# Kernel tuning notes

Hardware: AMD Instinct MI355X
Metric: run time of the kernel (lower is better)

Reference implementation:

```python
import jax, jax.numpy as jnp
import numpy as np

N_QUBITS = 10
DEPTH = 6
NUM_CLASSES = 16
BATCH = 65536

# PennyLane default.qubit convention: wire 0 is the most significant bit of the
# computational-basis index. State kept as (B, 2**n) complex64.

def _rot(state, w, n, c, s, is_ry):
    """Apply RX (is_ry=False) or RY (is_ry=True) with cos/sin of half-angle c,s
    (broadcastable to (B,1,1)) on wire w of an n-qubit batched state."""
    B = state.shape[0]
    st = state.reshape(B, 1 << w, 2, 1 << (n - 1 - w))
    a0, a1 = st[:, :, 0, :], st[:, :, 1, :]
    if is_ry:
        n0 = c * a0 - s * a1
        n1 = s * a0 + c * a1
    else:  # RX: [[c, -i s], [-i s, c]]
        n0 = c * a0 - 1j * s * a1
        n1 = -1j * s * a0 + c * a1
    return jnp.stack([n0, n1], axis=2).reshape(B, -1)


def _cz(state, w, n):
    """CZ on wires (w, w+1): negate amplitudes where both bits are 1."""
    B = state.shape[0]
    st = state.reshape(B, 1 << w, 2, 2, 1 << (n - 2 - w))
    st = st.at[:, :, 1, 1, :].multiply(-1.0)
    return st.reshape(B, -1)


def _expval_z(probs, w, n):
    B = probs.shape[0]
    p = probs.reshape(B, 1 << w, 2, 1 << (n - 1 - w))
    return (p[:, :, 0, :] - p[:, :, 1, :]).sum(axis=(1, 2))


def setup_inputs() -> dict:
    key = jax.random.key(0)
    k1, k2, k3, k4 = jax.random.split(key, 4)
    x = jax.random.normal(k1, (BATCH, N_QUBITS), dtype=jnp.float32)
    params = jax.random.normal(k2, (DEPTH, N_QUBITS), dtype=jnp.float32)
    bound = 1.0 / np.sqrt(N_QUBITS)
    w_cls = jax.random.uniform(k3, (NUM_CLASSES, N_QUBITS), minval=-bound, maxval=bound, dtype=jnp.float32)
    b_cls = jax.random.uniform(k4, (NUM_CLASSES,), minval=-bound, maxval=bound, dtype=jnp.float32)
    return {"x": x, "params": params, "w_cls": w_cls, "b_cls": b_cls}


def reference(x, params, w_cls, b_cls):
    B, n = x.shape[0], N_QUBITS
    state = jnp.zeros((B, 1 << n), dtype=jnp.complex64).at[:, 0].set(1.0)
    # Data encoding: RX(x[:, q]) on wire q (per-sample angles).
    for q in range(n):
        half = x[:, q] * 0.5
        c = jnp.cos(half)[:, None, None]
        s = jnp.sin(half)[:, None, None]
        state = _rot(state, q, n, c, s, is_ry=False)
    # Variational ansatz: per layer, RY(params[d, q]) then CZ ladder.
    for d in range(DEPTH):
        for q in range(n):
            half = params[d, q] * 0.5
            state = _rot(state, q, n, jnp.cos(half), jnp.sin(half), is_ry=True)
        for q in range(n - 1):
            state = _cz(state, q, n)
    probs = state.real ** 2 + state.imag ** 2  # (B, 2**n)
    exp = jnp.stack([_expval_z(probs, q, n) for q in range(n)], axis=1)  # (B, n)
    return exp @ w_cls.T + b_cls
```

## Files before the change

kernel.cpp:

```cpp
#include <hip/hip_runtime.h>
#include <math.h>


typedef unsigned int u32;
typedef _Float16 h2 __attribute__((ext_vector_type(2)));

constexpr int NQ = 10;
constexpr int NCLS = 16;
constexpr u32 SGN  = 0x80000000u;
constexpr u32 SGN2 = 0x80008000u;

__device__ __forceinline__ float i2f(int i) { return __builtin_bit_cast(float, i); }
__device__ __forceinline__ int   f2i(float f) { return __builtin_bit_cast(int, f); }
__device__ __forceinline__ u32   f2u(float f) { return __builtin_bit_cast(u32, f); }
__device__ __forceinline__ float u2f(u32 u)   { return __builtin_bit_cast(float, u); }
__device__ __forceinline__ u32   h2u(h2 v)    { return __builtin_bit_cast(u32, v); }
__device__ __forceinline__ h2    u2h(u32 u)   { return __builtin_bit_cast(h2, u); }

__device__ __forceinline__ h2 fma2(h2 a, h2 b, h2 c) {
    return __builtin_elementwise_fma(a, b, c);
}

template<int SWZ>
__device__ __forceinline__ h2 swzh(h2 v) {
    return u2h((u32)__builtin_amdgcn_ds_swizzle(__builtin_bit_cast(int, v), SWZ));
}
template<int SWZ>
__device__ __forceinline__ float swzf(float v) {
    return i2f(__builtin_amdgcn_ds_swizzle(f2i(v), SWZ));
}

constexpr int SW1 = 0x041F;
constexpr int SW2 = 0x081F;
constexpr int SW4 = 0x101F;
constexpr int SW8 = 0x201F;
#define GBC(q) (0x10 | ((q) << 5))

template<int SWZ>
__device__ __forceinline__ void cross_ry(h2 (&st)[64], h2 ts) {
#pragma unroll
    for (int r = 0; r < 64; ++r) st[r] = fma2(ts, swzh<SWZ>(st[r]), st[r]);
}

template<int B, int NB>
__device__ __forceinline__ void local_ry(h2 (&st)[64], h2 t) {
#pragma unroll
    for (int r0 = 0; r0 < 64; ++r0) {
        if ((r0 & (1 << B)) == 0) {
            const int r1 = r0 | (1 << B);
            const h2 a0 = st[r0], a1 = st[r1];
            if ((__builtin_popcount(r0 & NB) & 1) == 0) {
                st[r0] = fma2(t, -a1, a0);
                st[r1] = fma2(t,  a0, a1);
            } else {
                st[r0] = fma2(t,  a1, a0);
                st[r1] = fma2(t, -a0, a1);
            }
        }
    }
}

struct Sgn { u32 n0, m0, n1, m1, n2, m2, n3, m3, g4; };

template<bool MOD, bool GS>
__device__ __forceinline__ void ry_layer(h2 (&st)[64], const u32* __restrict__ tw,
                                         int base, int gi, const Sgn& sg) {
    { const h2 ts = u2h(tw[base + 0] ^ (MOD ? sg.m0 : sg.n0)); cross_ry<SW8>(st, ts); }
    { const h2 ts = u2h(tw[base + 1] ^ (MOD ? sg.m1 : sg.n1)); cross_ry<SW4>(st, ts); }
    { const h2 ts = u2h(tw[base + 2] ^ (MOD ? sg.m2 : sg.n2)); cross_ry<SW2>(st, ts); }
    {
        const h2 ts = u2h(tw[base + 3] ^ (MOD ? sg.m3 : sg.n3));
        if constexpr (MOD) {
            const h2 th = u2h(h2u(ts) ^ SGN2);
#pragma unroll
            for (int r = 0; r < 32; ++r)  st[r] = fma2(ts, swzh<SW1>(st[r]), st[r]);
#pragma unroll
            for (int r = 32; r < 64; ++r) st[r] = fma2(th, swzh<SW1>(st[r]), st[r]);
        } else {
            cross_ry<SW1>(st, ts);
        }
    }
    { const h2 t = u2h(tw[base + 4] ^ (MOD ? sg.g4 : 0u));
      local_ry<5, MOD ? 0x10 : 0>(st, t); }
    local_ry<4, MOD ? 0x28 : 0>(st, u2h(tw[base + 5]));
    local_ry<3, MOD ? 0x14 : 0>(st, u2h(tw[base + 6]));
    local_ry<2, MOD ? 0x0A : 0>(st, u2h(tw[base + 7]));
    local_ry<1, MOD ? 0x05 : 0>(st, u2h(tw[base + 8]));
    local_ry<0, MOD ? 0x02 : 0>(st, u2h(tw[base + 9]));
    if constexpr (GS) {
        const h2 g = u2h(tw[gi]);
#pragma unroll
        for (int r = 0; r < 64; ++r) st[r] = g * st[r];
    }
}

__global__ void __launch_bounds__(64) qnn_prep(const float* __restrict__ params,
                                               u32* __restrict__ ws) {
    const int l = threadIdx.x;
    if (l < 60) {
        float s, c;
        __sincosf(params[l] * 0.5f, &s, &c);
        const float t = s / c;
        const h2 t2 = { (_Float16)t, (_Float16)t };
        ws[l] = h2u(t2);
    }
    if (l < 3) {
        float g = 1.f;
        for (int k = 0; k < 20; ++k) g *= __cosf(params[l * 20 + k] * 0.5f);
        const h2 g2 = { (_Float16)g, (_Float16)g };
        ws[60 + l] = h2u(g2);
    }
}

__global__ void __launch_bounds__(256) qnn_kernel(
    const float* __restrict__ x,
    const u32*   __restrict__ tw,
    const float* __restrict__ w_cls,
    const float* __restrict__ b_cls,
    float* __restrict__ out,
    int batch)
{
    const int lane = threadIdx.x & 63;
    const int wid  = threadIdx.x >> 6;
    const int wave = blockIdx.x * (blockDim.x >> 6) + wid;
    const int g    = lane & 15;
    const int b    = wave * 4 + (lane >> 4);

    float cx, sx;
    { const int q = (g < NQ) ? g : 0; __sincosf(x[b * NQ + q] * 0.5f, &sx, &cx); }

#define BCQ(Q) const float c##Q = swzf<GBC(Q)>(cx), s##Q = swzf<GBC(Q)>(sx);
    BCQ(0) BCQ(1) BCQ(2) BCQ(3) BCQ(4) BCQ(5) BCQ(6) BCQ(7) BCQ(8) BCQ(9)
#undef BCQ

    Sgn sg;
    sg.n0 = (g & 8) ? 0 : SGN2;  sg.m0 = sg.n0 ^ ((g & 4) ? SGN2 : 0);
    sg.n1 = (g & 4) ? 0 : SGN2;  sg.m1 = sg.n1 ^ ((((g >> 3) ^ (g >> 1)) & 1) ? SGN2 : 0);
    sg.n2 = (g & 2) ? 0 : SGN2;  sg.m2 = sg.n2 ^ ((((g >> 2) ^ g) & 1) ? SGN2 : 0);
    sg.n3 = (g & 1) ? 0 : SGN2;  sg.m3 = sg.n3 ^ (((g >> 1) & 1) ? SGN2 : 0);
    sg.g4 = (g & 1) ? SGN2 : 0;

    float F = ((g >> 3) & 1 ? s0 : c0) * ((g >> 2) & 1 ? s1 : c1)
            * ((g >> 1) & 1 ? s2 : c2) * ((g & 1) ? s3 : c3);
    const int lpar = __popc(g & (g >> 1) & 0x7) & 1;
    F = u2f(f2u(F) ^ (u32(lpar) << 31));
    const float s4m = (g & 1) ? -s4 : s4;
    float uu[8], vv[8];
    {
        const float a0 = F * c4, a1 = F * s4m;
        const float b0 = c5, b1 = s5;
        const float t00 = a0 * b0, t01 = a0 * b1, t10 = a1 * b0, t11 = a1 * b1;
        uu[0] = t00 * c6; uu[1] = t00 * s6; uu[2] = t01 * c6; uu[3] = t01 * s6;
        uu[4] = t10 * c6; uu[5] = t10 * s6; uu[6] = t11 * c6; uu[7] = t11 * s6;
        const float p00 = c7 * c8, p01 = c7 * s8, p10 = s7 * c8, p11 = s7 * s8;
        vv[0] = p00 * c9; vv[1] = p00 * s9; vv[2] = p01 * c9; vv[3] = p01 * s9;
        vv[4] = p10 * c9; vv[5] = p10 * s9; vv[6] = p11 * c9; vv[7] = p11 * s9;
    }
    const int kl = __popc(g) & 3;
    const float pa = (kl == 0) ? 1.f : ((kl == 2) ? -1.f : 0.f);
    const float pb = (kl == 1) ? -1.f : ((kl == 3) ? 1.f : 0.f);
    const float phx[4] = {pa, pb, -pa, -pb};
    const float phy[4] = {pb, -pa, -pb, pa};

    h2 st[64];
#pragma unroll
    for (int r = 0; r < 64; ++r) {
        const float Ar = uu[r >> 3] * vv[r & 7];
        const int j = ((__popc(r) & 3) + 2 * (__popc(r & (r >> 1) & 0x1F) & 1)) & 3;
        st[r] = __builtin_bit_cast(h2, __builtin_amdgcn_cvt_pkrtz(Ar * phx[j], Ar * phy[j]));
    }

    ry_layer<true , false>(st, tw,  0,  0, sg);
    ry_layer<false, true >(st, tw, 10, 60, sg);
    ry_layer<true , false>(st, tw, 20,  0, sg);
    ry_layer<false, true >(st, tw, 30, 61, sg);
    ry_layer<true , false>(st, tw, 40,  0, sg);
    ry_layer<false, true >(st, tw, 50, 62, sg);

    float f4 = 0.f, f5 = 0.f, f6 = 0.f, f7 = 0.f, f8 = 0.f, f9 = 0.f, pt = 0.f;
#pragma unroll
    for (int i = 0; i < 8; ++i) {
        float p[8];
#pragma unroll
        for (int j = 0; j < 8; ++j)
            p[j] = __builtin_amdgcn_fdot2(st[8*i + j], st[8*i + j], 0.f, false);
        const float a0 = p[0] + p[1], a1 = p[2] + p[3];
        const float a2 = p[4] + p[5], a3 = p[6] + p[7];
        f9 += (p[0] - p[1]) + (p[2] - p[3]) + (p[4] - p[5]) + (p[6] - p[7]);
        const float b0 = a0 + a1, b1 = a2 + a3;
        f8 += (a0 - a1) + (a2 - a3);
        const float c = b0 + b1;
        f7 += b0 - b1;
        f6 += (i & 1) ? -c : c;
        f5 += (i & 2) ? -c : c;
        f4 += (i & 4) ? -c : c;
        pt += c;
    }

    h2 p45 = __builtin_bit_cast(h2, __builtin_amdgcn_cvt_pkrtz(f4, f5));
    h2 p67 = __builtin_bit_cast(h2, __builtin_amdgcn_cvt_pkrtz(f6, f7));
    h2 p89 = __builtin_bit_cast(h2, __builtin_amdgcn_cvt_pkrtz(f8, f9));
    p45 += swzh<SW1>(p45);  p67 += swzh<SW1>(p67);  p89 += swzh<SW1>(p89);
    p45 += swzh<SW2>(p45);  p67 += swzh<SW2>(p67);  p89 += swzh<SW2>(p89);
    p45 += swzh<SW4>(p45);  p67 += swzh<SW4>(p67);  p89 += swzh<SW4>(p89);
    p45 += swzh<SW8>(p45);  p67 += swzh<SW8>(p67);  p89 += swzh<SW8>(p89);
    const float g4v = (float)p45[0], g5v = (float)p45[1];
    const float g6v = (float)p67[0], g7v = (float)p67[1];
    const float g8v = (float)p89[0], g9v = (float)p89[1];

    float v = pt;
    {
        float p;
        p = swzf<SW1>(v);  v = p + u2f(f2u(v) ^ ((g & 1) ? SGN : 0u));
        p = swzf<SW2>(v);  v = p + u2f(f2u(v) ^ ((g & 2) ? SGN : 0u));
        p = swzf<SW4>(v);  v = p + u2f(f2u(v) ^ ((g & 4) ? SGN : 0u));
        p = swzf<SW8>(v);  v = p + u2f(f2u(v) ^ ((g & 8) ? SGN : 0u));
    }
    const float e0 = swzf<GBC(8)>(v);
    const float e1 = swzf<GBC(4)>(v);
    const float e2 = swzf<GBC(2)>(v);
    const float e3 = swzf<GBC(1)>(v);

    {
        const float* wr = w_cls + g * NQ;
        float dot = e0 * wr[0];
        dot = fmaf(e1,  wr[1], dot);
        dot = fmaf(e2,  wr[2], dot);
        dot = fmaf(e3,  wr[3], dot);
        dot = fmaf(g4v, wr[4], dot);
        dot = fmaf(g5v, wr[5], dot);
        dot = fmaf(g6v, wr[6], dot);
        dot = fmaf(g7v, wr[7], dot);
        dot = fmaf(g8v, wr[8], dot);
        dot = fmaf(g9v, wr[9], dot);
        out[b * NCLS + g] = dot + b_cls[g];
    }
}

extern "C" void kernel_launch(void* const* d_in, const int* in_sizes, int n_in,
                              void* d_out, int out_size, void* d_ws, size_t ws_size,
                              hipStream_t stream) {
    const float* x      = (const float*)d_in[0];
    const float* params = (const float*)d_in[1];
    const float* w_cls  = (const float*)d_in[2];
    const float* b_cls  = (const float*)d_in[3];
    float* out = (float*)d_out;
    u32*   ws  = (u32*)d_ws;

    const int batch = in_sizes[0] / NQ;
    const int WAVES_PER_BLOCK = 4;
    const int ELEMS_PER_BLOCK = WAVES_PER_BLOCK * 4;

    hipLaunchKernelGGL(qnn_prep, dim3(1), dim3(64), 0, stream, params, ws);

    dim3 block(64 * WAVES_PER_BLOCK);
    dim3 grid(batch / ELEMS_PER_BLOCK);
    hipLaunchKernelGGL(qnn_kernel, grid, block, 0, stream,
                       x, (const u32*)ws, w_cls, b_cls, out, batch);
}
```

Before: 160.0 us.

## Fold first RY layer into product-state encoding and merge normalization scales

The first variational RY layer acts on a product state before any CZ, so it is folded analytically into each qubit's complex single-qubit amplitudes (RY·RX computed per lane from precomputed cos/sin of params). This removes one full ry_layer pass over the 64-register state. In exchange the initial state build uses complex multiplies instead of real ones. The gain normalisations of the later layers are regrouped: one fp16 scale is applied inside a layer and the rest is applied as a squared fp32 factor on the probabilities, which changes rounding and fp16 range behaviour.

```diff
diff --git a/kernel.cpp b/kernel.cpp
--- a/kernel.cpp
+++ b/kernel.cpp
@@ -35,6 +35,12 @@
 constexpr int SW4 = 0x101F;
 constexpr int SW8 = 0x201F;
 #define GBC(q) (0x10 | ((q) << 5))
+
+struct c32 { float re, im; };
+__device__ __forceinline__ c32 cmul(c32 a, c32 b) {
+    return { fmaf(a.re, b.re, -(a.im * b.im)),
+             fmaf(a.re, b.im,  a.im * b.re) };
+}
 
 template<int SWZ>
 __device__ __forceinline__ void cross_ry(h2 (&st)[64], h2 ts) {
@@ -104,11 +110,20 @@
         const h2 t2 = { (_Float16)t, (_Float16)t };
         ws[l] = h2u(t2);
     }
-    if (l < 3) {
-        float g = 1.f;
-        for (int k = 0; k < 20; ++k) g *= __cosf(params[l * 20 + k] * 0.5f);
-        const h2 g2 = { (_Float16)g, (_Float16)g };
-        ws[60 + l] = h2u(g2);
+    if (l < 10) {
+        float s, c;
+        __sincosf(params[l] * 0.5f, &s, &c);
+        ws[64 + 2*l]     = f2u(c);
+        ws[64 + 2*l + 1] = f2u(s);
+    }
+    if (l == 0) {
+        float gA = 1.f;
+        for (int k = 10; k < 30; ++k) gA *= __cosf(params[k] * 0.5f);
+        const h2 g2 = { (_Float16)gA, (_Float16)gA };
+        ws[60] = h2u(g2);
+        float gB = 1.f;
+        for (int k = 30; k < 60; ++k) gB *= __cosf(params[k] * 0.5f);
+        ws[61] = f2u(gB * gB);
     }
 }
 
@@ -126,12 +141,20 @@
     const int g    = lane & 15;
     const int b    = wave * 4 + (lane >> 4);
 
-    float cx, sx;
-    { const int q = (g < NQ) ? g : 0; __sincosf(x[b * NQ + q] * 0.5f, &sx, &cx); }
-
-#define BCQ(Q) const float c##Q = swzf<GBC(Q)>(cx), s##Q = swzf<GBC(Q)>(sx);
-    BCQ(0) BCQ(1) BCQ(2) BCQ(3) BCQ(4) BCQ(5) BCQ(6) BCQ(7) BCQ(8) BCQ(9)
-#undef BCQ
+    float Are, Aim, Bre, Bim;
+    {
+        const int q = (g < NQ) ? g : 0;
+        float cxe, sxe;
+        __sincosf(x[b * NQ + q] * 0.5f, &sxe, &cxe);
+        const float ct = u2f(tw[64 + 2*q]), st_ = u2f(tw[64 + 2*q + 1]);
+        Are = ct * cxe;  Aim = st_ * sxe;
+        Bre = st_ * cxe; Bim = -(ct * sxe);
+    }
+
+#define BCW(Q) const float Ar##Q = swzf<GBC(Q)>(Are), Ai##Q = swzf<GBC(Q)>(Aim), \
+                           Br##Q = swzf<GBC(Q)>(Bre), Bi##Q = swzf<GBC(Q)>(Bim);
+    BCW(0) BCW(1) BCW(2) BCW(3) BCW(4) BCW(5) BCW(6) BCW(7) BCW(8) BCW(9)
+#undef BCW
 
     Sgn sg;
     sg.n0 = (g & 8) ? 0 : SGN2;  sg.m0 = sg.n0 ^ ((g & 4) ? SGN2 : 0);
@@ -140,42 +163,59 @@
     sg.n3 = (g & 1) ? 0 : SGN2;  sg.m3 = sg.n3 ^ (((g >> 1) & 1) ? SGN2 : 0);
     sg.g4 = (g & 1) ? SGN2 : 0;
 
-    float F = ((g >> 3) & 1 ? s0 : c0) * ((g >> 2) & 1 ? s1 : c1)
-            * ((g >> 1) & 1 ? s2 : c2) * ((g & 1) ? s3 : c3);
-    const int lpar = __popc(g & (g >> 1) & 0x7) & 1;
-    F = u2f(f2u(F) ^ (u32(lpar) << 31));
-    const float s4m = (g & 1) ? -s4 : s4;
-    float uu[8], vv[8];
-    {
-        const float a0 = F * c4, a1 = F * s4m;
-        const float b0 = c5, b1 = s5;
-        const float t00 = a0 * b0, t01 = a0 * b1, t10 = a1 * b0, t11 = a1 * b1;
-        uu[0] = t00 * c6; uu[1] = t00 * s6; uu[2] = t01 * c6; uu[3] = t01 * s6;
-        uu[4] = t10 * c6; uu[5] = t10 * s6; uu[6] = t11 * c6; uu[7] = t11 * s6;
-        const float p00 = c7 * c8, p01 = c7 * s8, p10 = s7 * c8, p11 = s7 * s8;
-        vv[0] = p00 * c9; vv[1] = p00 * s9; vv[2] = p01 * c9; vv[3] = p01 * s9;
-        vv[4] = p10 * c9; vv[5] = p10 * s9; vv[6] = p11 * c9; vv[7] = p11 * s9;
-    }
-    const int kl = __popc(g) & 3;
-    const float pa = (kl == 0) ? 1.f : ((kl == 2) ? -1.f : 0.f);
-    const float pb = (kl == 1) ? -1.f : ((kl == 3) ? 1.f : 0.f);
-    const float phx[4] = {pa, pb, -pa, -pb};
-    const float phy[4] = {pb, -pa, -pb, pa};
+    const c32 w0 = (g & 8) ? c32{Br0, Bi0} : c32{Ar0, Ai0};
+    const c32 w1 = (g & 4) ? c32{Br1, Bi1} : c32{Ar1, Ai1};
+    const c32 w2 = (g & 2) ? c32{Br2, Bi2} : c32{Ar2, Ai2};
+    const c32 w3 = (g & 1) ? c32{Br3, Bi3} : c32{Ar3, Ai3};
+    c32 F = cmul(cmul(w0, w1), cmul(w2, w3));
+    const u32 lps = (__popc(g & (g >> 1) & 0x7) & 1) ? SGN : 0;
+    F.re = u2f(f2u(F.re) ^ lps);
+    F.im = u2f(f2u(F.im) ^ lps);
+
+    const u32 bs = (g & 1) ? SGN : 0;
+    const c32 a4 = {Ar4, Ai4};
+    const c32 b4 = {u2f(f2u(Br4) ^ bs), u2f(f2u(Bi4) ^ bs)};
+
+    c32 uu[8];
+    {
+        const c32 u0 = cmul(F, a4), u1 = cmul(F, b4);
+        const c32 a5 = {Ar5, Ai5}, b5 = {Br5, Bi5};
+        const c32 t00 = cmul(u0, a5), t01 = cmul(u0, b5);
+        const c32 t10 = cmul(u1, a5), t11 = cmul(u1, b5);
+        const c32 a6 = {Ar6, Ai6}, b6 = {Br6, Bi6};
+        uu[0] = cmul(t00, a6); uu[1] = cmul(t00, b6);
+        uu[2] = cmul(t01, a6); uu[3] = cmul(t01, b6);
+        uu[4] = cmul(t10, a6); uu[5] = cmul(t10, b6);
+        uu[6] = cmul(t11, a6); uu[7] = cmul(t11, b6);
+    }
+    c32 vv[8];
+    {
+        const c32 a7 = {Ar7, Ai7}, b7 = {Br7, Bi7};
+        const c32 a8 = {Ar8, Ai8}, b8 = {Br8, Bi8};
+        const c32 q00 = cmul(a7, a8), q01 = cmul(a7, b8);
+        const c32 q10 = cmul(b7, a8), q11 = cmul(b7, b8);
+        const c32 a9 = {Ar9, Ai9}, b9 = {Br9, Bi9};
+        vv[0] = cmul(q00, a9); vv[1] = cmul(q00, b9);
+        vv[2] = cmul(q01, a9); vv[3] = cmul(q01, b9);
+        vv[4] = cmul(q10, a9); vv[5] = cmul(q10, b9);
+        vv[6] = cmul(q11, a9); vv[7] = cmul(q11, b9);
+    }
 
     h2 st[64];
 #pragma unroll
     for (int r = 0; r < 64; ++r) {
-        const float Ar = uu[r >> 3] * vv[r & 7];
-        const int j = ((__popc(r) & 3) + 2 * (__popc(r & (r >> 1) & 0x1F) & 1)) & 3;
-        st[r] = __builtin_bit_cast(h2, __builtin_amdgcn_cvt_pkrtz(Ar * phx[j], Ar * phy[j]));
-    }
-
-    ry_layer<true , false>(st, tw,  0,  0, sg);
-    ry_layer<false, true >(st, tw, 10, 60, sg);
-    ry_layer<true , false>(st, tw, 20,  0, sg);
-    ry_layer<false, true >(st, tw, 30, 61, sg);
+        const c32 m = cmul(uu[r >> 3], vv[r & 7]);
+        if (__popc(r & (r >> 1) & 0x1F) & 1)
+            st[r] = __builtin_bit_cast(h2, __builtin_amdgcn_cvt_pkrtz(-m.re, -m.im));
+        else
+            st[r] = __builtin_bit_cast(h2, __builtin_amdgcn_cvt_pkrtz(m.re, m.im));
+    }
+
+    ry_layer<false, false>(st, tw, 10,  0, sg);
+    ry_layer<true , true >(st, tw, 20, 60, sg);
+    ry_layer<false, false>(st, tw, 30,  0, sg);
     ry_layer<true , false>(st, tw, 40,  0, sg);
-    ry_layer<false, true >(st, tw, 50, 62, sg);
+    ry_layer<false, false>(st, tw, 50,  0, sg);
 
     float f4 = 0.f, f5 = 0.f, f6 = 0.f, f7 = 0.f, f8 = 0.f, f9 = 0.f, pt = 0.f;
 #pragma unroll
@@ -197,6 +237,12 @@
         pt += c;
     }
 
+    {
+        const float gB2 = u2f(tw[61]);
+        f4 *= gB2; f5 *= gB2; f6 *= gB2; f7 *= gB2;
+        f8 *= gB2; f9 *= gB2; pt *= gB2;
+    }
+
     h2 p45 = __builtin_bit_cast(h2, __builtin_amdgcn_cvt_pkrtz(f4, f5));
     h2 p67 = __builtin_bit_cast(h2, __builtin_amdgcn_cvt_pkrtz(f6, f7));
     h2 p89 = __builtin_bit_cast(h2, __builtin_amdgcn_cvt_pkrtz(f8, f9));
```

Measured after the change: 142.0 us. 11.2% less time.
